# Kernel tuning notes

Measured on AMD Instinct MI355X. Metric: run time of the kernel, lower is better.

Reference implementation:

```python
import jax, jax.numpy as jnp
import numpy as np


def setup_inputs() -> dict:
    key = jax.random.key(0)
    k1, k2, k3, k4, k5 = jax.random.split(key, 5)
    B, S, D, H, L = 32, 2048, 512, 32, 2
    inp = jax.random.normal(k1, (B, S, D), dtype=jnp.float32)
    mask = jax.random.randint(k2, (B, S), 0, 2) > 0  # bool [B,S]
    projector = jax.random.normal(k3, (D, H), dtype=jnp.float32) * 0.05
    hidden = jax.random.normal(k4, (L - 1, H, H), dtype=jnp.float32) * 0.05
    evaluator = jax.random.normal(k5, (H, 1), dtype=jnp.float32) * 0.05
    return {"inp": inp, "mask": mask, "projector": projector,
            "hidden": hidden, "evaluator": evaluator}


def reference(inp, mask, projector, hidden, evaluator):
    act = jax.nn.sigmoid
    scale = jnp.asarray(projector.shape[-1], inp.dtype) ** 0.5  # sqrt(hidden_dim)
    m = mask.astype(inp.dtype)[..., None]          # [B,S,1]
    x = inp * m                                     # masked inputs (inp *= mask)
    w = act(jnp.einsum('bsd,dh->bsh', x, projector) / scale)
    for i in range(hidden.shape[0]):                # n_layers - 1 hidden matmuls
        w = act(jnp.einsum('bsh,hk->bsk', w, hidden[i]) / scale)
    w = act(jnp.einsum('bsh,ho->bso', w, evaluator) / scale)  # [B,S,1]
    w = jax.nn.softmax(w, axis=-2)                  # softmax over sequence axis
    w = w * m
    w = w / (jnp.sum(w, axis=1, keepdims=True) + 1e-12)
    return jnp.sum(w * x, axis=1)                   # [B,D]
```

## Files before the change

### kernel.cpp

```cpp
#include <hip/hip_runtime.h>

#define B_   32
#define S_   2048
#define D_   512
#define H_   32
#define BS_  (B_*S_)
#define INV_SCALE 0.17677669529663689f


typedef short  s16x8 __attribute__((ext_vector_type(8)));
typedef float  f32x4 __attribute__((ext_vector_type(4)));

__device__ __forceinline__ float sigmoidf_(float x) {
    return 1.0f / (1.0f + __expf(-x));
}

__device__ __forceinline__ unsigned short f2bf(float f) {
    unsigned u = __float_as_uint(f);
    u += 0x7fffu + ((u >> 16) & 1u);
    return (unsigned short)(u >> 16);
}

__global__ void kTransposeBf(const float* __restrict__ P, unsigned short* __restrict__ PTbf) {
    int o = blockIdx.x * 256 + threadIdx.x;
    int j = o >> 9, d = o & 511;
    PTbf[o] = f2bf(P[d * H_ + j]);
}

#define XST 520
#define WST 36

__global__ __launch_bounds__(256, 4) void kFused(
        const float* __restrict__ inp, const int* __restrict__ mask,
        const unsigned short* __restrict__ PTbf, const float* __restrict__ hd,
        const float* __restrict__ ev,
        float* __restrict__ partial, float2* __restrict__ zdm) {
    __shared__ __align__(16) unsigned short xs[32 * XST];
    __shared__ __align__(16) float w0f[32 * WST];
    __shared__ float cs[32];
    __shared__ float es[32];
    __shared__ float msk[32];

    const int tid = threadIdx.x;
    const int blk = blockIdx.x;
    const int rowBase = blk * 32;

    if (tid < 32) msk[tid] = (mask[rowBase + tid] != 0) ? 1.0f : 0.0f;

    const float4* g = (const float4*)inp + (size_t)rowBase * 128;
    float4 tmp[16];
    #pragma unroll
    for (int i = 0; i < 16; ++i)
        tmp[i] = g[i * 256 + tid];
    #pragma unroll
    for (int i = 0; i < 16; ++i) {
        int fi = i * 256 + tid;
        int row = fi >> 7, kq = fi & 127;
        unsigned p0, p1;
        asm("v_cvt_pk_bf16_f32 %0, %1, %2" : "=v"(p0) : "v"(tmp[i].x), "v"(tmp[i].y));
        asm("v_cvt_pk_bf16_f32 %0, %1, %2" : "=v"(p1) : "v"(tmp[i].z), "v"(tmp[i].w));
        uint2 u; u.x = p0; u.y = p1;
        *(uint2*)(xs + row * XST + kq * 4) = u;
    }
    __syncthreads();

    const int wave = tid >> 6, lane = tid & 63;
    const int rt = wave & 1, ct = wave >> 1;
    const int m = lane & 15, quad = lane >> 4;

    const unsigned short* arow = xs + (rt * 16 + m) * XST + quad * 8;
    const unsigned short* brow = PTbf + (size_t)(ct * 16 + m) * 512 + quad * 8;

    f32x4 acc = {0.f, 0.f, 0.f, 0.f};
    #pragma unroll
    for (int ks = 0; ks < 16; ++ks) {
        s16x8 a = *(const s16x8*)(arow + ks * 32);
        s16x8 b = *(const s16x8*)(brow + ks * 32);
        acc = __builtin_amdgcn_mfma_f32_16x16x32_bf16(a, b, acc, 0, 0, 0);
    }

    #pragma unroll
    for (int r = 0; r < 4; ++r) {
        int rowL = rt * 16 + quad * 4 + r;
        w0f[rowL * WST + ct * 16 + m] = sigmoidf_(msk[rowL] * acc[r] * INV_SCALE);
    }
    __syncthreads();

    {
        const int k = tid & 31, slot = tid >> 5;
        const float evk = ev[k];
        float hdv[32];
        #pragma unroll
        for (int j = 0; j < 32; ++j) hdv[j] = hd[j * 32 + k];

        #pragma unroll
        for (int t = 0; t < 4; ++t) {
            const int row = slot + 8 * t;
            const float4* wr = (const float4*)(w0f + row * WST);
            float s = 0.f;
            #pragma unroll
            for (int i = 0; i < 8; ++i) {
                float4 w4 = wr[i];
                s = fmaf(w4.x, hdv[4 * i + 0], s);
                s = fmaf(w4.y, hdv[4 * i + 1], s);
                s = fmaf(w4.z, hdv[4 * i + 2], s);
                s = fmaf(w4.w, hdv[4 * i + 3], s);
            }
            float val = sigmoidf_(s * INV_SCALE) * evk;
            #pragma unroll
            for (int o = 1; o < 32; o <<= 1)
                val += __shfl_xor(val, o);
            if (k == 0) {
                float v2 = sigmoidf_(val * INV_SCALE);
                float e  = __expf(v2);
                es[row] = e;
                cs[row] = msk[row] * e;
            }
        }
    }
    __syncthreads();

    if (tid < 64) {
        float z = 0.f, dm = 0.f;
        if (tid < 32) { z = es[tid]; dm = cs[tid]; }
        #pragma unroll
        for (int o = 32; o > 0; o >>= 1) {
            z  += __shfl_down(z, o);
            dm += __shfl_down(dm, o);
        }
        if (tid == 0) zdm[blk] = make_float2(z, dm);
    }

    float a0 = 0.f, a1 = 0.f;
    #pragma unroll 8
    for (int row = 0; row < 32; ++row) {
        unsigned u = *(const unsigned*)(xs + row * XST + 2 * tid);
        float x0 = __uint_as_float(u << 16);
        float x1 = __uint_as_float(u & 0xffff0000u);
        float c = cs[row];
        a0 = fmaf(c, x0, a0);
        a1 = fmaf(c, x1, a1);
    }
    ((float2*)(partial + (size_t)blk * 512))[tid] = make_float2(a0, a1);
}

__global__ __launch_bounds__(256) void kReduce(
        const float* __restrict__ partial, const float2* __restrict__ zdm,
        float* __restrict__ out) {
    const int b = blockIdx.x, tid = threadIdx.x;
    __shared__ float sInv;

    if (tid < 64) {
        float2 p = zdm[b * 64 + tid];
        float z = p.x, dm = p.y;
        #pragma unroll
        for (int o = 32; o > 0; o >>= 1) {
            z  += __shfl_down(z, o);
            dm += __shfl_down(dm, o);
        }
        if (tid == 0) sInv = 1.0f / (dm + 1e-12f * z);
    }
    __syncthreads();

    const float2* pp = (const float2*)partial + (size_t)b * 64 * 256 + tid;
    float a0 = 0.f, b0 = 0.f, a1 = 0.f, b1 = 0.f;
    float a2 = 0.f, b2 = 0.f, a3 = 0.f, b3 = 0.f;
    #pragma unroll
    for (int i = 0; i < 64; i += 4) {
        float2 p0 = pp[(size_t)(i + 0) * 256];
        float2 p1 = pp[(size_t)(i + 1) * 256];
        float2 p2 = pp[(size_t)(i + 2) * 256];
        float2 p3 = pp[(size_t)(i + 3) * 256];
        a0 += p0.x; b0 += p0.y; a1 += p1.x; b1 += p1.y;
        a2 += p2.x; b2 += p2.y; a3 += p3.x; b3 += p3.y;
    }
    const float inv = sInv;
    float2 r;
    r.x = ((a0 + a1) + (a2 + a3)) * inv;
    r.y = ((b0 + b1) + (b2 + b3)) * inv;
    ((float2*)out)[b * 256 + tid] = r;
}

extern "C" void kernel_launch(void* const* d_in, const int* in_sizes, int n_in,
                              void* d_out, int out_size, void* d_ws, size_t ws_size,
                              hipStream_t stream) {
    const float* inp  = (const float*)d_in[0];
    const int*   mask = (const int*)d_in[1];
    const float* proj = (const float*)d_in[2];
    const float* hid  = (const float*)d_in[3];
    const float* ev   = (const float*)d_in[4];
    float* out = (float*)d_out;

    unsigned short* PTbf = (unsigned short*)d_ws;
    float2* zdm     = (float2*)((char*)d_ws + 32768);
    float*  partial = (float*)((char*)d_ws + 49152);

    kTransposeBf<<<64, 256, 0, stream>>>(proj, PTbf);
    kFused      <<<BS_ / 32, 256, 0, stream>>>(inp, mask, PTbf, hid, ev, partial, zdm);
    kReduce     <<<B_, 256, 0, stream>>>(partial, zdm, out);
}
```

Baseline: 213.8 us.

## Process four row tiles per block with register-prefetched next tile

Each block now loops over four 32-row tiles instead of one, quartering the grid. The projector B-fragments and the hidden/evaluator weights are loaded into registers once per block and reused across tiles. The next tile's fp32 input is prefetched into registers while the current tile's MFMA and epilogue run. The cost is higher register pressure: launch bounds drop to 2 blocks per CU, and there is an extra barrier per tile, which may reduce occupancy and latency hiding on a memory-bound kernel.

```diff
diff --git a/kernel.cpp b/kernel.cpp
--- a/kernel.cpp
+++ b/kernel.cpp
@@ -1,10 +1,14 @@
 #include <hip/hip_runtime.h>
+
 
 #define B_   32
 #define S_   2048
 #define D_   512
 #define H_   32
 #define BS_  (B_*S_)
+#define NTILE_ (BS_/32)
+#define TPB_   4
+#define GRID_  (NTILE_/TPB_)
 #define INV_SCALE 0.17677669529663689f
 
 
@@ -30,7 +34,7 @@
 #define XST 520
 #define WST 36
 
-__global__ __launch_bounds__(256, 4) void kFused(
+__global__ __launch_bounds__(256, 2) void kFused(
         const float* __restrict__ inp, const int* __restrict__ mask,
         const unsigned short* __restrict__ PTbf, const float* __restrict__ hd,
         const float* __restrict__ ev,
@@ -42,60 +46,75 @@
     __shared__ float msk[32];
 
     const int tid = threadIdx.x;
-    const int blk = blockIdx.x;
-    const int rowBase = blk * 32;
-
-    if (tid < 32) msk[tid] = (mask[rowBase + tid] != 0) ? 1.0f : 0.0f;
-
-    const float4* g = (const float4*)inp + (size_t)rowBase * 128;
-    float4 tmp[16];
-    #pragma unroll
-    for (int i = 0; i < 16; ++i)
-        tmp[i] = g[i * 256 + tid];
-    #pragma unroll
-    for (int i = 0; i < 16; ++i) {
-        int fi = i * 256 + tid;
-        int row = fi >> 7, kq = fi & 127;
-        unsigned p0, p1;
-        asm("v_cvt_pk_bf16_f32 %0, %1, %2" : "=v"(p0) : "v"(tmp[i].x), "v"(tmp[i].y));
-        asm("v_cvt_pk_bf16_f32 %0, %1, %2" : "=v"(p1) : "v"(tmp[i].z), "v"(tmp[i].w));
-        uint2 u; u.x = p0; u.y = p1;
-        *(uint2*)(xs + row * XST + kq * 4) = u;
-    }
-    __syncthreads();
-
     const int wave = tid >> 6, lane = tid & 63;
     const int rt = wave & 1, ct = wave >> 1;
     const int m = lane & 15, quad = lane >> 4;
 
-    const unsigned short* arow = xs + (rt * 16 + m) * XST + quad * 8;
-    const unsigned short* brow = PTbf + (size_t)(ct * 16 + m) * 512 + quad * 8;
-
-    f32x4 acc = {0.f, 0.f, 0.f, 0.f};
+    s16x8 bf[16];
+    {
+        const unsigned short* brow = PTbf + (size_t)(ct * 16 + m) * 512 + quad * 8;
+        #pragma unroll
+        for (int ks = 0; ks < 16; ++ks)
+            bf[ks] = *(const s16x8*)(brow + ks * 32);
+    }
+    const int k = tid & 31, slot = tid >> 5;
+    float hdv[32];
     #pragma unroll
-    for (int ks = 0; ks < 16; ++ks) {
-        s16x8 a = *(const s16x8*)(arow + ks * 32);
-        s16x8 b = *(const s16x8*)(brow + ks * 32);
-        acc = __builtin_amdgcn_mfma_f32_16x16x32_bf16(a, b, acc, 0, 0, 0);
-    }
-
-    #pragma unroll
-    for (int r = 0; r < 4; ++r) {
-        int rowL = rt * 16 + quad * 4 + r;
-        w0f[rowL * WST + ct * 16 + m] = sigmoidf_(msk[rowL] * acc[r] * INV_SCALE);
-    }
-    __syncthreads();
-
+    for (int j = 0; j < 32; ++j) hdv[j] = hd[j * 32 + k];
+    const float evk = ev[k];
+
+    const int tile0 = blockIdx.x * TPB_;
+
+    float4 tmp[16];
     {
-        const int k = tid & 31, slot = tid >> 5;
-        const float evk = ev[k];
-        float hdv[32];
-        #pragma unroll
-        for (int j = 0; j < 32; ++j) hdv[j] = hd[j * 32 + k];
-
-        #pragma unroll
-        for (int t = 0; t < 4; ++t) {
-            const int row = slot + 8 * t;
+        const float4* g = (const float4*)inp + (size_t)tile0 * 4096;
+        #pragma unroll
+        for (int i = 0; i < 16; ++i)
+            tmp[i] = g[i * 256 + tid];
+    }
+
+    for (int t = 0; t < TPB_; ++t) {
+        const int tile = tile0 + t;
+        const int rowBase = tile * 32;
+
+        #pragma unroll
+        for (int i = 0; i < 16; ++i) {
+            int fi = i * 256 + tid;
+            int row = fi >> 7, kq = fi & 127;
+            unsigned p0, p1;
+            asm("v_cvt_pk_bf16_f32 %0, %1, %2" : "=v"(p0) : "v"(tmp[i].x), "v"(tmp[i].y));
+            asm("v_cvt_pk_bf16_f32 %0, %1, %2" : "=v"(p1) : "v"(tmp[i].z), "v"(tmp[i].w));
+            uint2 u; u.x = p0; u.y = p1;
+            *(uint2*)(xs + row * XST + kq * 4) = u;
+        }
+        if (tid < 32) msk[tid] = (mask[rowBase + tid] != 0) ? 1.0f : 0.0f;
+        __syncthreads();
+
+        if (t + 1 < TPB_) {
+            const float4* g2 = (const float4*)inp + (size_t)(tile + 1) * 4096;
+            #pragma unroll
+            for (int i = 0; i < 16; ++i)
+                tmp[i] = g2[i * 256 + tid];
+        }
+
+        const unsigned short* arow = xs + (rt * 16 + m) * XST + quad * 8;
+        f32x4 acc = {0.f, 0.f, 0.f, 0.f};
+        #pragma unroll
+        for (int ks = 0; ks < 16; ++ks) {
+            s16x8 a = *(const s16x8*)(arow + ks * 32);
+            acc = __builtin_amdgcn_mfma_f32_16x16x32_bf16(a, bf[ks], acc, 0, 0, 0);
+        }
+
+        #pragma unroll
+        for (int r = 0; r < 4; ++r) {
+            int rowL = rt * 16 + quad * 4 + r;
+            w0f[rowL * WST + ct * 16 + m] = sigmoidf_(msk[rowL] * acc[r] * INV_SCALE);
+        }
+        __syncthreads();
+
+        #pragma unroll
+        for (int tt = 0; tt < 4; ++tt) {
+            const int row = slot + 8 * tt;
             const float4* wr = (const float4*)(w0f + row * WST);
             float s = 0.f;
             #pragma unroll
@@ -117,31 +136,33 @@
                 cs[row] = msk[row] * e;
             }
         }
-    }
-    __syncthreads();
-
-    if (tid < 64) {
-        float z = 0.f, dm = 0.f;
-        if (tid < 32) { z = es[tid]; dm = cs[tid]; }
-        #pragma unroll
-        for (int o = 32; o > 0; o >>= 1) {
-            z  += __shfl_down(z, o);
-            dm += __shfl_down(dm, o);
-        }
-        if (tid == 0) zdm[blk] = make_float2(z, dm);
-    }
-
-    float a0 = 0.f, a1 = 0.f;
-    #pragma unroll 8
-    for (int row = 0; row < 32; ++row) {
-        unsigned u = *(const unsigned*)(xs + row * XST + 2 * tid);
-        float x0 = __uint_as_float(u << 16);
-        float x1 = __uint_as_float(u & 0xffff0000u);
-        float c = cs[row];
-        a0 = fmaf(c, x0, a0);
-        a1 = fmaf(c, x1, a1);
-    }
-    ((float2*)(partial + (size_t)blk * 512))[tid] = make_float2(a0, a1);
+        __syncthreads();
+
+        if (tid < 64) {
+            float z = 0.f, dm = 0.f;
+            if (tid < 32) { z = es[tid]; dm = cs[tid]; }
+            #pragma unroll
+            for (int o = 32; o > 0; o >>= 1) {
+                z  += __shfl_down(z, o);
+                dm += __shfl_down(dm, o);
+            }
+            if (tid == 0) zdm[tile] = make_float2(z, dm);
+        }
+
+        float a0 = 0.f, a1 = 0.f;
+        #pragma unroll 8
+        for (int row = 0; row < 32; ++row) {
+            unsigned u = *(const unsigned*)(xs + row * XST + 2 * tid);
+            float x0 = __uint_as_float(u << 16);
+            float x1 = __uint_as_float(u & 0xffff0000u);
+            float c = cs[row];
+            a0 = fmaf(c, x0, a0);
+            a1 = fmaf(c, x1, a1);
+        }
+        ((float2*)(partial + (size_t)tile * 512))[tid] = make_float2(a0, a1);
+
+        __syncthreads();
+    }
 }
 
 __global__ __launch_bounds__(256) void kReduce(
@@ -196,6 +217,6 @@
     float*  partial = (float*)((char*)d_ws + 49152);
 
     kTransposeBf<<<64, 256, 0, stream>>>(proj, PTbf);
-    kFused      <<<BS_ / 32, 256, 0, stream>>>(inp, mask, PTbf, hid, ev, partial, zdm);
+    kFused      <<<GRID_, 256, 0, stream>>>(inp, mask, PTbf, hid, ev, partial, zdm);
     kReduce     <<<B_, 256, 0, stream>>>(partial, zdm, out);
 }
```

Result: faster. 207.9 us (-2.7%).
